# Performance work log

Measured on AMD Instinct MI355X. Metric: run time of the kernel, lower is better.

The kernel has to match this reference:

```python
import jax, jax.numpy as jnp
import numpy as np
from jax import lax

V, E, NL, NS, DC, EX = 32000, 1024, 4, 16, 4, 2
DI = EX * E          # 2048 inner dim
DTR = E // 16        # 64 dt_rank
BSZ, L = 2, 512
EPS = 1e-5


def setup_inputs() -> dict:
    key = jax.random.key(0)
    ks = jax.random.split(key, 12)
    s = 0.02
    emb = jax.random.normal(ks[0], (V, E), jnp.float32) * s
    ln_w = jnp.ones((NL, E), jnp.float32)
    ln_b = jnp.zeros((NL, E), jnp.float32)
    in_proj_w = jax.random.normal(ks[1], (NL, 2 * DI, E), jnp.float32) * s
    conv_w = jax.random.normal(ks[2], (NL, DI, DC), jnp.float32) * 0.1
    conv_b = jnp.zeros((NL, DI), jnp.float32)
    x_proj_w = jax.random.normal(ks[3], (NL, DTR + 2 * NS, DI), jnp.float32) * s
    dt_proj_w = jax.random.normal(ks[4], (NL, DI, DTR), jnp.float32) * s
    dt_proj_b = jax.random.normal(ks[5], (NL, DI), jnp.float32) * 0.1
    # canonical S4D-real init: A[d,n] = n+1  ->  A_log = log(A)
    A_log = jnp.log(jnp.tile(jnp.arange(1, NS + 1, dtype=jnp.float32)[None, None, :], (NL, DI, 1)))
    D_param = jnp.ones((NL, DI), jnp.float32)
    out_proj_w = jax.random.normal(ks[6], (NL, E, DI), jnp.float32) * s
    fln_w = jnp.ones((E,), jnp.float32)
    fln_b = jnp.zeros((E,), jnp.float32)
    input_ids = jax.random.randint(ks[7], (BSZ, L), 0, V, jnp.int64)
    targets = jax.random.randint(ks[8], (BSZ, L), 0, V, jnp.int64)
    return dict(input_ids=input_ids, targets=targets, emb=emb, ln_w=ln_w, ln_b=ln_b,
                in_proj_w=in_proj_w, conv_w=conv_w, conv_b=conv_b, x_proj_w=x_proj_w,
                dt_proj_w=dt_proj_w, dt_proj_b=dt_proj_b, A_log=A_log, D_param=D_param,
                out_proj_w=out_proj_w, fln_w=fln_w, fln_b=fln_b)


def _layer_norm(x, w, b):
    mu = x.mean(-1, keepdims=True)
    var = ((x - mu) ** 2).mean(-1, keepdims=True)
    return (x - mu) * lax.rsqrt(var + EPS) * w + b


def _mamba_block(x, in_w, cw, cb, xw, dtw, dtb, a_log, d_par, ow):
    # x: (B,L,E)
    xz = jnp.einsum('ble,fe->blf', x, in_w)          # (B,L,2*DI)
    u, res = jnp.split(xz, 2, axis=-1)               # each (B,L,DI)
    # causal depthwise conv1d, kernel width DC (left pad DC-1)
    u_pad = jnp.pad(u, ((0, 0), (DC - 1, 0), (0, 0)))
    u_conv = sum(cw[:, k] * u_pad[:, k:k + u.shape[1], :] for k in range(DC))
    u = jax.nn.silu(u_conv + cb)
    x_dbl = jnp.einsum('bld,fd->blf', u, xw)         # (B,L,DTR+2*NS)
    dt = x_dbl[..., :DTR]
    Bm = x_dbl[..., DTR:DTR + NS]                    # (B,L,NS)
    Cm = x_dbl[..., DTR + NS:]                       # (B,L,NS)
    delta = jax.nn.softplus(jnp.einsum('blr,dr->bld', dt, dtw) + dtb)  # (B,L,DI)
    A = -jnp.exp(a_log)                              # (DI,NS)
    dA = jnp.exp(delta[..., None] * A)               # (B,L,DI,NS)
    dBu = delta[..., None] * Bm[:, :, None, :] * u[..., None]

    def step(h, inp):
        dA_t, dBu_t, C_t = inp
        h = dA_t * h + dBu_t                         # (B,DI,NS)
        y = jnp.einsum('bdn,bn->bd', h, C_t)
        return h, y

    h0 = jnp.zeros((x.shape[0], DI, NS), x.dtype)
    _, ys = lax.scan(step, h0, (dA.transpose(1, 0, 2, 3), dBu.transpose(1, 0, 2, 3), Cm.transpose(1, 0, 2)))
    y = ys.transpose(1, 0, 2) + u * d_par            # (B,L,DI)
    y = y * jax.nn.silu(res)
    return jnp.einsum('bld,ed->ble', y, ow)


def reference(input_ids, targets, emb, ln_w, ln_b, in_proj_w, conv_w, conv_b,
              x_proj_w, dt_proj_w, dt_proj_b, A_log, D_param, out_proj_w, fln_w, fln_b):
    x = emb[input_ids]                               # (B,L,E)
    for l in range(NL):
        h = _layer_norm(x, ln_w[l], ln_b[l])
        h = _mamba_block(h, in_proj_w[l], conv_w[l], conv_b[l], x_proj_w[l],
                         dt_proj_w[l], dt_proj_b[l], A_log[l], D_param[l], out_proj_w[l])
        x = x + h
    x = _layer_norm(x, fln_w, fln_b)
    logits = jnp.einsum('ble,ve->blv', x, emb)       # tied lm_head
    logp = jax.nn.log_softmax(logits, axis=-1)
    valid = targets != -1
    safe_t = jnp.where(valid, targets, 0)
    nll = -jnp.take_along_axis(logp, safe_t[..., None], axis=-1)[..., 0]
    loss = jnp.where(valid, nll, 0.0).mean()
    return logits, loss
```

## Files before the change

kernel.cpp:

```cpp
#include <hip/hip_runtime.h>
#include <cstdint>
#include <cstddef>

#define L_SEQ 512
#define NBATCH 2
#define NTOK 1024
#define E_DIM 1024
#define V_DIM 32000
#define DI_DIM 2048
#define NS_DIM 16
#define DTR_DIM 64
#define DC_DIM 4
#define NL_DIM 4
#define NC 8
#define LC (L_SEQ / NC)

typedef __bf16 bf16;
typedef __bf16 bf16x8 __attribute__((ext_vector_type(8)));
typedef __bf16 bf16x4 __attribute__((ext_vector_type(4)));
typedef float  f32x4  __attribute__((ext_vector_type(4)));

__device__ __forceinline__ void gload_lds16(const void* g, void* l)
{
    __builtin_amdgcn_global_load_lds((const __attribute__((address_space(1))) uint32_t*)g,
                                     (__attribute__((address_space(3))) uint32_t*)l, 16, 0, 0);
}

__device__ __forceinline__ float softplusf(float z)
{
    return fmaxf(z, 0.0f) + log1pf(expf(-fabsf(z)));
}

__global__ void cast_f32_to_bf16(const float* __restrict__ in, bf16* __restrict__ out, int n4)
{
    int stride = gridDim.x * blockDim.x;
    for (int i = blockIdx.x * blockDim.x + threadIdx.x; i < n4; i += stride) {
        f32x4 v = ((const f32x4*)in)[i];
        bf16x4 o;
        o[0] = (bf16)v[0]; o[1] = (bf16)v[1]; o[2] = (bf16)v[2]; o[3] = (bf16)v[3];
        ((bf16x4*)out)[i] = o;
    }
}

__global__ void cast3_kernel(const float* __restrict__ a, bf16* __restrict__ oa, int na4,
                             const float* __restrict__ b, bf16* __restrict__ ob, int nb4,
                             const float* __restrict__ c, bf16* __restrict__ oc, int nc4)
{
    int stride = gridDim.x * blockDim.x;
    int tot = na4 + nb4 + nc4;
    for (int i = blockIdx.x * blockDim.x + threadIdx.x; i < tot; i += stride) {
        const float* src; bf16* dst; int k = i;
        if (k < na4) { src = a; dst = oa; }
        else if ((k -= na4) < nb4) { src = b; dst = ob; }
        else { k -= nb4; src = c; dst = oc; }
        f32x4 v = ((const f32x4*)src)[k];
        bf16x4 o;
        o[0] = (bf16)v[0]; o[1] = (bf16)v[1]; o[2] = (bf16)v[2]; o[3] = (bf16)v[3];
        ((bf16x4*)dst)[k] = o;
    }
}

__global__ void embed_kernel(const int* __restrict__ ids, const float* __restrict__ emb,
                             float* __restrict__ x)
{
    int t = blockIdx.x;
    int id = ids[t];
    ((f32x4*)(x + (size_t)t * E_DIM))[threadIdx.x] =
        ((const f32x4*)(emb + (size_t)id * E_DIM))[threadIdx.x];
}

__global__ void ln_kernel(const float* __restrict__ x, const float* __restrict__ w,
                          const float* __restrict__ b, bf16* __restrict__ out)
{
    int t = blockIdx.x;
    int tid = threadIdx.x;
    f32x4 v = ((const f32x4*)(x + (size_t)t * E_DIM))[tid];
    float s  = v[0] + v[1] + v[2] + v[3];
    float sq = v[0]*v[0] + v[1]*v[1] + v[2]*v[2] + v[3]*v[3];
#pragma unroll
    for (int off = 1; off < 64; off <<= 1) { s += __shfl_xor(s, off); sq += __shfl_xor(sq, off); }
    __shared__ float ps[4], pq[4];
    if ((tid & 63) == 0) { ps[tid >> 6] = s; pq[tid >> 6] = sq; }
    __syncthreads();
    float S  = ps[0] + ps[1] + ps[2] + ps[3];
    float SQ = pq[0] + pq[1] + pq[2] + pq[3];
    float mu  = S * (1.0f / E_DIM);
    float var = SQ * (1.0f / E_DIM) - mu * mu;
    float rs  = rsqrtf(var + 1e-5f);
    f32x4 wv = ((const f32x4*)w)[tid];
    f32x4 bv = ((const f32x4*)b)[tid];
    bf16x4 o;
#pragma unroll
    for (int i = 0; i < 4; ++i) o[i] = (bf16)((v[i] - mu) * rs * wv[i] + bv[i]);
    ((bf16x4*)(out + (size_t)t * E_DIM))[tid] = o;
}

template<int BM, int BN, int MODE>
__global__ __launch_bounds__(256) void gemm_bt(const bf16* __restrict__ A, const bf16* __restrict__ B,
                                               void* __restrict__ Cv, int K,
                                               int lda, int ldb, int ldc,
                                               const float* __restrict__ bias,
                                               int RB, int CB, int CBpad)
{
    int pid = blockIdx.x;
    int xcd = pid & 7;
    int j   = pid >> 3;
    int cpx = CBpad >> 3;
    int rb  = j % RB;
    int cb  = xcd * cpx + j / RB;
    if (cb >= CB) return;

    __shared__ __align__(16) bf16 As[BM * 32];
    __shared__ __align__(16) bf16 Bs[BN * 32];
    int tid  = threadIdx.x;
    int lane = tid & 63;
    int wid  = tid >> 6;
    int wr = wid >> 1, wc = wid & 1;
    int li = lane & 15, lg = lane >> 4;
    const bf16* Ablk = A + (size_t)(rb * BM) * lda;
    const bf16* Bblk = B + (size_t)(cb * BN) * ldb;
    constexpr int MR  = BM / 32;
    constexpr int NR  = BN / 32;
    constexpr int TOT = (BM + BN) * 4;
    f32x4 acc[MR][NR] = {};
    for (int k0 = 0; k0 < K; k0 += 32) {
        __syncthreads();
#pragma unroll
        for (int it = 0; it < TOT / 256; ++it) {
            int wbase = it * 256 + wid * 64;
            int idx   = wbase + lane;
            if (wbase < BM * 4) {
                int row = idx >> 2, seg = idx & 3;
                gload_lds16(Ablk + (size_t)row * lda + k0 + seg * 8, As + (size_t)wbase * 8);
            } else {
                int bb  = wbase - BM * 4;
                int bi  = bb + lane;
                int row = bi >> 2, seg = bi & 3;
                gload_lds16(Bblk + (size_t)row * ldb + k0 + seg * 8, Bs + (size_t)bb * 8);
            }
        }
        __syncthreads();
        bf16x8 af[MR], bfr[NR];
#pragma unroll
        for (int m = 0; m < MR; ++m) af[m]  = *(const bf16x8*)&As[(wr * (BM/2) + m * 16 + li) * 32 + lg * 8];
#pragma unroll
        for (int n = 0; n < NR; ++n) bfr[n] = *(const bf16x8*)&Bs[(wc * (BN/2) + n * 16 + li) * 32 + lg * 8];
#pragma unroll
        for (int m = 0; m < MR; ++m)
#pragma unroll
            for (int n = 0; n < NR; ++n)
                acc[m][n] = __builtin_amdgcn_mfma_f32_16x16x32_bf16(af[m], bfr[n], acc[m][n], 0, 0, 0);
    }
    int row0 = rb * BM + wr * (BM/2);
    int col0 = cb * BN + wc * (BN/2);
    float* Cf = (float*)Cv;
    bf16*  Cb = (bf16*)Cv;
#pragma unroll
    for (int m = 0; m < MR; ++m) {
#pragma unroll
        for (int n = 0; n < NR; ++n) {
            int r = row0 + m * 16 + lg * 4;
            int c = col0 + n * 16 + li;
#pragma unroll
            for (int q = 0; q < 4; ++q) {
                float v = acc[m][n][q];
                if (MODE == 0) {
                    Cf[(size_t)(r + q) * ldc + c] = v;
                } else if (MODE == 1) {
                    float* cp = Cf + (size_t)(r + q) * ldc + c;
                    *cp = v + *cp;
                } else if (MODE == 2) {
                    Cb[(size_t)(r + q) * ldc + c] = (bf16)softplusf(v + bias[c]);
                } else if (MODE == 4) {
                    Cb[(size_t)(r + q) * ldc + c] = (bf16)v;
                }
            }
        }
    }
}

template<int BM, int BN, int MODE>
static void launch_gemm(const bf16* A, const bf16* B, void* C, int M, int N, int K,
                        int lda, int ldb, int ldc, const float* bias, hipStream_t stream)
{
    int RB = M / BM;
    int CB = (N + BN - 1) / BN;
    int CBpad = (CB + 7) & ~7;
    gemm_bt<BM, BN, MODE><<<RB * CBpad, 256, 0, stream>>>(A, B, C, K, lda, ldb, ldc,
                                                          bias, RB, CB, CBpad);
}

__global__ __launch_bounds__(256) void cxk_kernel(
        const bf16* __restrict__ xz, const float* __restrict__ cw,
        const float* __restrict__ cb, const float* __restrict__ xw,
        float* __restrict__ xdbl, bf16* __restrict__ dt_bf, bf16* __restrict__ u_bf)
{
    int t0  = blockIdx.x * 2;
    int bb  = t0 >> 9;
    int tid = threadIdx.x;
    int f   = tid & 127;
    int ks  = tid >> 7;
    __shared__ __align__(16) float sxz[5][256];
    __shared__ __align__(16) float su[2][256];
    __shared__ float pacc[2][128];
    float acc[2] = {0, 0};
    for (int kc = 0; kc < DI_DIM; kc += 256) {
        __syncthreads();
#pragma unroll
        for (int it = 0; it < 2; ++it) {
            int idx = it * 256 + tid;
            if (idx < 320) {
                int row = idx >> 6, c4 = (idx & 63) * 4;
                int tr = t0 - 3 + row;
                float v0 = 0, v1 = 0, v2 = 0, v3 = 0;
                if (tr >= bb * L_SEQ) {
                    bf16x4 v = *(const bf16x4*)&xz[(size_t)tr * (2 * DI_DIM) + kc + c4];
                    v0 = (float)v[0]; v1 = (float)v[1]; v2 = (float)v[2]; v3 = (float)v[3];
                }
                sxz[row][c4] = v0; sxz[row][c4 + 1] = v1;
                sxz[row][c4 + 2] = v2; sxz[row][c4 + 3] = v3;
            }
        }
        __syncthreads();
        {
            int c = tid;
            const float* cwp = cw + (size_t)(kc + c) * DC_DIM;
            float w0 = cwp[0], w1 = cwp[1], w2 = cwp[2], w3 = cwp[3];
            float bs = cb[kc + c];
#pragma unroll
            for (int tt = 0; tt < 2; ++tt) {
                float a = bs + w0 * sxz[tt][c] + w1 * sxz[tt + 1][c]
                             + w2 * sxz[tt + 2][c] + w3 * sxz[tt + 3][c];
                float uo = a / (1.0f + __expf(-a));
                su[tt][c] = uo;
                u_bf[(size_t)(t0 + tt) * DI_DIM + kc + c] = (bf16)uo;
            }
        }
        __syncthreads();
        if (f < 96) {
            int kb = ks * 128;
            for (int kk = kb; kk < kb + 128; kk += 4) {
                f32x4 wv = *(const f32x4*)&xw[(size_t)f * DI_DIM + kc + kk];
#pragma unroll
                for (int tt = 0; tt < 2; ++tt) {
                    f32x4 uv = *(f32x4*)&su[tt][kk];
                    acc[tt] += wv[0]*uv[0] + wv[1]*uv[1] + wv[2]*uv[2] + wv[3]*uv[3];
                }
            }
        }
    }
    if (ks == 1 && f < 96) {
#pragma unroll
        for (int tt = 0; tt < 2; ++tt) pacc[tt][f] = acc[tt];
    }
    __syncthreads();
    if (ks == 0 && f < 96) {
#pragma unroll
        for (int tt = 0; tt < 2; ++tt) {
            float v = acc[tt] + pacc[tt][f];
            xdbl[(size_t)(t0 + tt) * 96 + f] = v;
            if (f < 64) dt_bf[(size_t)(t0 + tt) * DTR_DIM + f] = (bf16)v;
        }
    }
}

__global__ __launch_bounds__(256) void scan_phase_a(
        const bf16* __restrict__ delta, const float* __restrict__ xdbl,
        const bf16* __restrict__ u_bf, const float* __restrict__ A_log,
        float* __restrict__ Pbuf, float* __restrict__ Sbuf)
{
    int tid = threadIdx.x;
    int c   = blockIdx.x & (NC - 1);
    int dblk= (blockIdx.x >> 3) & 127;
    int b   = blockIdx.x >> 10;
    int d0  = dblk << 4;
    int n = tid & 15, dl = tid >> 4;
    int d = d0 + dl;
    float Ac = -expf(A_log[(size_t)d * NS_DIM + n]);
    float h = 0.0f, P = 1.0f;
    __shared__ float s_dlt[32][16], s_u[32][16], s_B[32][16];
    int tt0 = tid >> 4, cc = tid & 15;
    int tbase = b * L_SEQ + c * LC;
    for (int t0 = 0; t0 < LC; t0 += 32) {
        __syncthreads();
#pragma unroll
        for (int jj = 0; jj < 2; ++jj) {
            int tt = jj * 16 + tt0;
            size_t trow = (size_t)(tbase + t0 + tt);
            s_dlt[tt][cc] = (float)delta[trow * DI_DIM + d0 + cc];
            s_u[tt][cc]   = (float)u_bf[trow * DI_DIM + d0 + cc];
            s_B[tt][cc]   = xdbl[trow * 96 + 64 + cc];
        }
        __syncthreads();
#pragma unroll
        for (int t = 0; t < 32; ++t) {
            float dlt = s_dlt[t][dl];
            float dA  = __expf(dlt * Ac);
            h = fmaf(dA, h, dlt * s_B[t][n] * s_u[t][dl]);
            P *= dA;
        }
    }
    size_t oi = (((size_t)(b * NC + c) * DI_DIM) + d) * NS_DIM + n;
    Pbuf[oi] = P;
    Sbuf[oi] = h;
}

__global__ void scan_combine(const float* __restrict__ Pbuf, const float* __restrict__ Sbuf,
                             float* __restrict__ Hstart)
{
    int i  = blockIdx.x * 256 + threadIdx.x;
    int b  = i >> 15;
    int dn = i & 32767;
    float h = 0.0f;
#pragma unroll
    for (int c = 0; c < NC; ++c) {
        size_t oi = ((size_t)(b * NC + c) * (DI_DIM * NS_DIM)) + dn;
        Hstart[oi] = h;
        h = fmaf(Pbuf[oi], h, Sbuf[oi]);
    }
}

__global__ __launch_bounds__(256) void scan_phase_c(
        const bf16* __restrict__ delta, const float* __restrict__ xdbl,
        const bf16* __restrict__ u_bf, const bf16* __restrict__ xz,
        const float* __restrict__ A_log, const float* __restrict__ D_par,
        const float* __restrict__ Hstart, bf16* __restrict__ y)
{
    int tid = threadIdx.x;
    int c   = blockIdx.x & (NC - 1);
    int dblk= (blockIdx.x >> 3) & 127;
    int b   = blockIdx.x >> 10;
    int d0  = dblk << 4;
    int n = tid & 15, dl = tid >> 4;
    int d = d0 + dl;
    float Ac = -expf(A_log[(size_t)d * NS_DIM + n]);
    float Dp = D_par[d];
    float h = Hstart[(((size_t)(b * NC + c) * DI_DIM) + d) * NS_DIM + n];
    __shared__ float s_dlt[32][16], s_u[32][16], s_res[32][16], s_B[32][16], s_C[32][16];
    __shared__ bf16  s_y[32][16];
    int tt0 = tid >> 4, cc = tid & 15;
    int tbase = b * L_SEQ + c * LC;
    for (int t0 = 0; t0 < LC; t0 += 32) {
        __syncthreads();
#pragma unroll
        for (int jj = 0; jj < 2; ++jj) {
            int tt = jj * 16 + tt0;
            size_t trow = (size_t)(tbase + t0 + tt);
            s_dlt[tt][cc] = (float)delta[trow * DI_DIM + d0 + cc];
            s_u[tt][cc]   = (float)u_bf[trow * DI_DIM + d0 + cc];
            s_res[tt][cc] = (float)xz[trow * (2 * DI_DIM) + DI_DIM + d0 + cc];
            s_B[tt][cc]   = xdbl[trow * 96 + 64 + cc];
            s_C[tt][cc]   = xdbl[trow * 96 + 80 + cc];
        }
        __syncthreads();
#pragma unroll
        for (int t = 0; t < 32; ++t) {
            float dlt = s_dlt[t][dl];
            float uu  = s_u[t][dl];
            float dA  = __expf(dlt * Ac);
            float dBu = dlt * s_B[t][n] * uu;
            h = fmaf(dA, h, dBu);
            float yp = h * s_C[t][n];
            yp += __shfl_xor(yp, 1);
            yp += __shfl_xor(yp, 2);
            yp += __shfl_xor(yp, 4);
            yp += __shfl_xor(yp, 8);
            if (n == 0) {
                float res = s_res[t][dl];
                float yv  = fmaf(uu, Dp, yp) * (res / (1.0f + __expf(-res)));
                s_y[t][dl] = (bf16)yv;
            }
        }
        __syncthreads();
#pragma unroll
        for (int jj = 0; jj < 2; ++jj) {
            int tt = jj * 16 + tt0;
            size_t trow = (size_t)(tbase + t0 + tt);
            y[trow * DI_DIM + d0 + cc] = s_y[tt][cc];
        }
    }
}

__global__ void lse_nll_kernel(const float* __restrict__ logits, const int* __restrict__ targets,
                               float* __restrict__ lossp)
{
    int t = blockIdx.x, tid = threadIdx.x;
    const f32x4* row = (const f32x4*)(logits + (size_t)t * V_DIM);
    float m = -1e30f, s = 0.0f;
    for (int i = tid; i < V_DIM / 4; i += 256) {
        f32x4 v = row[i];
        float m4 = fmaxf(fmaxf(v[0], v[1]), fmaxf(v[2], v[3]));
        if (m4 > m) { s *= __expf(m - m4); m = m4; }
        s += __expf(v[0] - m) + __expf(v[1] - m) + __expf(v[2] - m) + __expf(v[3] - m);
    }
#pragma unroll
    for (int off = 1; off < 64; off <<= 1) {
        float mo = __shfl_xor(m, off), so = __shfl_xor(s, off);
        float nm = fmaxf(m, mo);
        s = s * __expf(m - nm) + so * __expf(mo - nm);
        m = nm;
    }
    __shared__ float pm[4], ps2[4];
    if ((tid & 63) == 0) { pm[tid >> 6] = m; ps2[tid >> 6] = s; }
    __syncthreads();
    if (tid == 0) {
        float M = fmaxf(fmaxf(pm[0], pm[1]), fmaxf(pm[2], pm[3]));
        float S = ps2[0] * __expf(pm[0] - M) + ps2[1] * __expf(pm[1] - M)
                + ps2[2] * __expf(pm[2] - M) + ps2[3] * __expf(pm[3] - M);
        int tg = targets[t];
        if (tg >= 0) {
            float v = (M + logf(S)) - logits[(size_t)t * V_DIM + tg];
            atomicAdd(lossp, v * (1.0f / NTOK));
        }
    }
}

extern "C" void kernel_launch(void* const* d_in, const int* in_sizes, int n_in,
                              void* d_out, int out_size, void* d_ws, size_t ws_size,
                              hipStream_t stream)
{
    const int*   ids   = (const int*)d_in[0];
    const int*   tgt   = (const int*)d_in[1];
    const float* emb   = (const float*)d_in[2];
    const float* ln_w  = (const float*)d_in[3];
    const float* ln_b  = (const float*)d_in[4];
    const float* inw   = (const float*)d_in[5];
    const float* convw = (const float*)d_in[6];
    const float* convb = (const float*)d_in[7];
    const float* xw    = (const float*)d_in[8];
    const float* dtw   = (const float*)d_in[9];
    const float* dtb   = (const float*)d_in[10];
    const float* alog  = (const float*)d_in[11];
    const float* dpar  = (const float*)d_in[12];
    const float* outw  = (const float*)d_in[13];
    const float* flnw  = (const float*)d_in[14];
    const float* flnb  = (const float*)d_in[15];
    float* logits = (float*)d_out;
    float* lossp  = logits + (size_t)NTOK * V_DIM;

    char* wsp = (char*)d_ws;
    size_t off = 0;
    auto alloc = [&](size_t bytes) -> void* {
        void* p = wsp + off;
        off += (bytes + 255) & ~(size_t)255;
        return p;
    };
    bf16*  emb_bf  = (bf16*)alloc((size_t)V_DIM * E_DIM * 2);
    bf16*  winl    = (bf16*)alloc((size_t)2 * DI_DIM * E_DIM * 2);
    bf16*  woutl   = (bf16*)alloc((size_t)E_DIM * DI_DIM * 2);
    bf16*  wdtl    = (bf16*)alloc((size_t)DI_DIM * DTR_DIM * 2);
    float* x       = (float*)alloc((size_t)NTOK * E_DIM * 4);
    bf16*  h_bf    = (bf16*)alloc((size_t)NTOK * E_DIM * 2);
    bf16*  xzb     = (bf16*)alloc((size_t)NTOK * 2 * DI_DIM * 2);
    bf16*  u_bf    = (bf16*)alloc((size_t)NTOK * DI_DIM * 2);
    float* xdbl    = (float*)alloc((size_t)NTOK * 96 * 4);
    bf16*  dt_bf   = (bf16*)alloc((size_t)NTOK * DTR_DIM * 2);
    bf16*  deltab  = (bf16*)alloc((size_t)NTOK * DI_DIM * 2);
    bf16*  y_bf    = (bf16*)alloc((size_t)NTOK * DI_DIM * 2);
    bf16*  xf_bf   = (bf16*)alloc((size_t)NTOK * E_DIM * 2);
    float* Pbuf    = (float*)alloc((size_t)NBATCH * NC * DI_DIM * NS_DIM * 4);
    float* Sbuf    = (float*)alloc((size_t)NBATCH * NC * DI_DIM * NS_DIM * 4);
    float* Hstart  = (float*)alloc((size_t)NBATCH * NC * DI_DIM * NS_DIM * 4);
    if (off > ws_size) return;

    hipMemsetAsync(lossp, 0, sizeof(float), stream);
    {
        int n4 = (int)((size_t)V_DIM * E_DIM / 4);
        cast_f32_to_bf16<<<4096, 256, 0, stream>>>(emb, emb_bf, n4);
    }
    embed_kernel<<<NTOK, 256, 0, stream>>>(ids, emb, x);

    for (int l = 0; l < NL_DIM; ++l) {
        cast3_kernel<<<2048, 256, 0, stream>>>(
            inw  + (size_t)l * 2 * DI_DIM * E_DIM, winl,  (int)((size_t)2 * DI_DIM * E_DIM / 4),
            outw + (size_t)l * E_DIM * DI_DIM,     woutl, (int)((size_t)E_DIM * DI_DIM / 4),
            dtw  + (size_t)l * DI_DIM * DTR_DIM,   wdtl,  (int)((size_t)DI_DIM * DTR_DIM / 4));

        ln_kernel<<<NTOK, 256, 0, stream>>>(x, ln_w + l * E_DIM, ln_b + l * E_DIM, h_bf);
        launch_gemm<128, 64, 4>(h_bf, winl, xzb, NTOK, 2 * DI_DIM, E_DIM,
                                E_DIM, E_DIM, 2 * DI_DIM, nullptr, stream);
        cxk_kernel<<<NTOK / 2, 256, 0, stream>>>(
            xzb, convw + (size_t)l * DI_DIM * DC_DIM, convb + (size_t)l * DI_DIM,
            xw + (size_t)l * 96 * DI_DIM, xdbl, dt_bf, u_bf);
        launch_gemm<64, 64, 2>(dt_bf, wdtl, deltab, NTOK, DI_DIM, DTR_DIM,
                               DTR_DIM, DTR_DIM, DI_DIM, dtb + (size_t)l * DI_DIM, stream);
        scan_phase_a<<<NBATCH * (DI_DIM / 16) * NC, 256, 0, stream>>>(
            deltab, xdbl, u_bf, alog + (size_t)l * DI_DIM * NS_DIM, Pbuf, Sbuf);
        scan_combine<<<NBATCH * DI_DIM * NS_DIM / 256, 256, 0, stream>>>(Pbuf, Sbuf, Hstart);
        scan_phase_c<<<NBATCH * (DI_DIM / 16) * NC, 256, 0, stream>>>(
            deltab, xdbl, u_bf, xzb, alog + (size_t)l * DI_DIM * NS_DIM,
            dpar + (size_t)l * DI_DIM, Hstart, y_bf);
        launch_gemm<64, 64, 1>(y_bf, woutl, x, NTOK, E_DIM, DI_DIM,
                               DI_DIM, DI_DIM, E_DIM, nullptr, stream);
    }
    ln_kernel<<<NTOK, 256, 0, stream>>>(x, flnw, flnb, xf_bf);
    launch_gemm<128, 128, 0>(xf_bf, emb_bf, logits, NTOK, V_DIM, E_DIM,
                             E_DIM, E_DIM, V_DIM, nullptr, stream);
    lse_nll_kernel<<<NTOK, 256, 0, stream>>>(logits, tgt, lossp);
}
```

Measured before the change: 921.5 us.

## Split-K out_proj with atomics, fold scan combine into phase C, widen conv tile

```diff
diff --git a/kernel.cpp b/kernel.cpp
--- a/kernel.cpp
+++ b/kernel.cpp
@@ -95,7 +95,7 @@
     ((bf16x4*)(out + (size_t)t * E_DIM))[tid] = o;
 }
 
-template<int BM, int BN, int MODE>
+template<int BM, int BN, int MODE, int SK>
 __global__ __launch_bounds__(256) void gemm_bt(const bf16* __restrict__ A, const bf16* __restrict__ B,
                                                void* __restrict__ Cv, int K,
                                                int lda, int ldb, int ldc,
@@ -103,12 +103,18 @@
                                                int RB, int CB, int CBpad)
 {
     int pid = blockIdx.x;
-    int xcd = pid & 7;
-    int j   = pid >> 3;
+    int per = RB * CBpad;
+    int sk  = pid / per;
+    int rem = pid - sk * per;
+    int xcd = rem & 7;
+    int j   = rem >> 3;
     int cpx = CBpad >> 3;
     int rb  = j % RB;
     int cb  = xcd * cpx + j / RB;
     if (cb >= CB) return;
+    int kseg = K / SK;
+    int kbeg = sk * kseg;
+    int kend = kbeg + kseg;
 
     __shared__ __align__(16) bf16 As[BM * 32];
     __shared__ __align__(16) bf16 Bs[BN * 32];
@@ -123,7 +129,7 @@
     constexpr int NR  = BN / 32;
     constexpr int TOT = (BM + BN) * 4;
     f32x4 acc[MR][NR] = {};
-    for (int k0 = 0; k0 < K; k0 += 32) {
+    for (int k0 = kbeg; k0 < kend; k0 += 32) {
         __syncthreads();
 #pragma unroll
         for (int it = 0; it < TOT / 256; ++it) {
@@ -173,21 +179,23 @@
                     Cb[(size_t)(r + q) * ldc + c] = (bf16)softplusf(v + bias[c]);
                 } else if (MODE == 4) {
                     Cb[(size_t)(r + q) * ldc + c] = (bf16)v;
+                } else if (MODE == 5) {
+                    atomicAdd(Cf + (size_t)(r + q) * ldc + c, v);
                 }
             }
         }
     }
 }
 
-template<int BM, int BN, int MODE>
+template<int BM, int BN, int MODE, int SK = 1>
 static void launch_gemm(const bf16* A, const bf16* B, void* C, int M, int N, int K,
                         int lda, int ldb, int ldc, const float* bias, hipStream_t stream)
 {
     int RB = M / BM;
     int CB = (N + BN - 1) / BN;
     int CBpad = (CB + 7) & ~7;
-    gemm_bt<BM, BN, MODE><<<RB * CBpad, 256, 0, stream>>>(A, B, C, K, lda, ldb, ldc,
-                                                          bias, RB, CB, CBpad);
+    gemm_bt<BM, BN, MODE, SK><<<RB * CBpad * SK, 256, 0, stream>>>(A, B, C, K, lda, ldb, ldc,
+                                                                   bias, RB, CB, CBpad);
 }
 
 __global__ __launch_bounds__(256) void cxk_kernel(
@@ -195,31 +203,28 @@
         const float* __restrict__ cb, const float* __restrict__ xw,
         float* __restrict__ xdbl, bf16* __restrict__ dt_bf, bf16* __restrict__ u_bf)
 {
-    int t0  = blockIdx.x * 2;
+    int t0  = blockIdx.x * 4;
     int bb  = t0 >> 9;
     int tid = threadIdx.x;
     int f   = tid & 127;
     int ks  = tid >> 7;
-    __shared__ __align__(16) float sxz[5][256];
-    __shared__ __align__(16) float su[2][256];
-    __shared__ float pacc[2][128];
-    float acc[2] = {0, 0};
+    __shared__ __align__(16) float sxz[7][256];
+    __shared__ __align__(16) float su[4][256];
+    __shared__ float pacc[4][128];
+    float acc[4] = {0, 0, 0, 0};
     for (int kc = 0; kc < DI_DIM; kc += 256) {
         __syncthreads();
-#pragma unroll
-        for (int it = 0; it < 2; ++it) {
-            int idx = it * 256 + tid;
-            if (idx < 320) {
-                int row = idx >> 6, c4 = (idx & 63) * 4;
-                int tr = t0 - 3 + row;
-                float v0 = 0, v1 = 0, v2 = 0, v3 = 0;
-                if (tr >= bb * L_SEQ) {
-                    bf16x4 v = *(const bf16x4*)&xz[(size_t)tr * (2 * DI_DIM) + kc + c4];
-                    v0 = (float)v[0]; v1 = (float)v[1]; v2 = (float)v[2]; v3 = (float)v[3];
-                }
-                sxz[row][c4] = v0; sxz[row][c4 + 1] = v1;
-                sxz[row][c4 + 2] = v2; sxz[row][c4 + 3] = v3;
-            }
+        if (tid < 224) {
+            int row = tid >> 5, c8 = (tid & 31) * 8;
+            int tr = t0 - 3 + row;
+            float vals[8] = {0, 0, 0, 0, 0, 0, 0, 0};
+            if (tr >= bb * L_SEQ) {
+                bf16x8 v = *(const bf16x8*)&xz[(size_t)tr * (2 * DI_DIM) + kc + c8];
+#pragma unroll
+                for (int jj = 0; jj < 8; ++jj) vals[jj] = (float)v[jj];
+            }
+#pragma unroll
+            for (int jj = 0; jj < 8; ++jj) sxz[row][c8 + jj] = vals[jj];
         }
         __syncthreads();
         {
@@ -228,7 +233,7 @@
             float w0 = cwp[0], w1 = cwp[1], w2 = cwp[2], w3 = cwp[3];
             float bs = cb[kc + c];
 #pragma unroll
-            for (int tt = 0; tt < 2; ++tt) {
+            for (int tt = 0; tt < 4; ++tt) {
                 float a = bs + w0 * sxz[tt][c] + w1 * sxz[tt + 1][c]
                              + w2 * sxz[tt + 2][c] + w3 * sxz[tt + 3][c];
                 float uo = a / (1.0f + __expf(-a));
@@ -242,7 +247,7 @@
             for (int kk = kb; kk < kb + 128; kk += 4) {
                 f32x4 wv = *(const f32x4*)&xw[(size_t)f * DI_DIM + kc + kk];
 #pragma unroll
-                for (int tt = 0; tt < 2; ++tt) {
+                for (int tt = 0; tt < 4; ++tt) {
                     f32x4 uv = *(f32x4*)&su[tt][kk];
                     acc[tt] += wv[0]*uv[0] + wv[1]*uv[1] + wv[2]*uv[2] + wv[3]*uv[3];
                 }
@@ -251,12 +256,12 @@
     }
     if (ks == 1 && f < 96) {
 #pragma unroll
-        for (int tt = 0; tt < 2; ++tt) pacc[tt][f] = acc[tt];
+        for (int tt = 0; tt < 4; ++tt) pacc[tt][f] = acc[tt];
     }
     __syncthreads();
     if (ks == 0 && f < 96) {
 #pragma unroll
-        for (int tt = 0; tt < 2; ++tt) {
+        for (int tt = 0; tt < 4; ++tt) {
             float v = acc[tt] + pacc[tt][f];
             xdbl[(size_t)(t0 + tt) * 96 + f] = v;
             if (f < 64) dt_bf[(size_t)(t0 + tt) * DTR_DIM + f] = (bf16)v;
@@ -305,26 +310,12 @@
     Sbuf[oi] = h;
 }
 
-__global__ void scan_combine(const float* __restrict__ Pbuf, const float* __restrict__ Sbuf,
-                             float* __restrict__ Hstart)
-{
-    int i  = blockIdx.x * 256 + threadIdx.x;
-    int b  = i >> 15;
-    int dn = i & 32767;
-    float h = 0.0f;
-#pragma unroll
-    for (int c = 0; c < NC; ++c) {
-        size_t oi = ((size_t)(b * NC + c) * (DI_DIM * NS_DIM)) + dn;
-        Hstart[oi] = h;
-        h = fmaf(Pbuf[oi], h, Sbuf[oi]);
-    }
-}
-
 __global__ __launch_bounds__(256) void scan_phase_c(
         const bf16* __restrict__ delta, const float* __restrict__ xdbl,
         const bf16* __restrict__ u_bf, const bf16* __restrict__ xz,
         const float* __restrict__ A_log, const float* __restrict__ D_par,
-        const float* __restrict__ Hstart, bf16* __restrict__ y)
+        const float* __restrict__ Pbuf, const float* __restrict__ Sbuf,
+        bf16* __restrict__ y)
 {
     int tid = threadIdx.x;
     int c   = blockIdx.x & (NC - 1);
@@ -335,7 +326,11 @@
     int d = d0 + dl;
     float Ac = -expf(A_log[(size_t)d * NS_DIM + n]);
     float Dp = D_par[d];
-    float h = Hstart[(((size_t)(b * NC + c) * DI_DIM) + d) * NS_DIM + n];
+    float h = 0.0f;
+    for (int cp = 0; cp < c; ++cp) {
+        size_t oi = (((size_t)(b * NC + cp) * DI_DIM) + d) * NS_DIM + n;
+        h = fmaf(Pbuf[oi], h, Sbuf[oi]);
+    }
     __shared__ float s_dlt[32][16], s_u[32][16], s_res[32][16], s_B[32][16], s_C[32][16];
     __shared__ bf16  s_y[32][16];
     int tt0 = tid >> 4, cc = tid & 15;
@@ -460,7 +455,6 @@
     bf16*  xf_bf   = (bf16*)alloc((size_t)NTOK * E_DIM * 2);
     float* Pbuf    = (float*)alloc((size_t)NBATCH * NC * DI_DIM * NS_DIM * 4);
     float* Sbuf    = (float*)alloc((size_t)NBATCH * NC * DI_DIM * NS_DIM * 4);
-    float* Hstart  = (float*)alloc((size_t)NBATCH * NC * DI_DIM * NS_DIM * 4);
     if (off > ws_size) return;
 
     hipMemsetAsync(lossp, 0, sizeof(float), stream);
@@ -479,19 +473,18 @@
         ln_kernel<<<NTOK, 256, 0, stream>>>(x, ln_w + l * E_DIM, ln_b + l * E_DIM, h_bf);
         launch_gemm<128, 64, 4>(h_bf, winl, xzb, NTOK, 2 * DI_DIM, E_DIM,
                                 E_DIM, E_DIM, 2 * DI_DIM, nullptr, stream);
-        cxk_kernel<<<NTOK / 2, 256, 0, stream>>>(
+        cxk_kernel<<<NTOK / 4, 256, 0, stream>>>(
             xzb, convw + (size_t)l * DI_DIM * DC_DIM, convb + (size_t)l * DI_DIM,
             xw + (size_t)l * 96 * DI_DIM, xdbl, dt_bf, u_bf);
         launch_gemm<64, 64, 2>(dt_bf, wdtl, deltab, NTOK, DI_DIM, DTR_DIM,
                                DTR_DIM, DTR_DIM, DI_DIM, dtb + (size_t)l * DI_DIM, stream);
         scan_phase_a<<<NBATCH * (DI_DIM / 16) * NC, 256, 0, stream>>>(
             deltab, xdbl, u_bf, alog + (size_t)l * DI_DIM * NS_DIM, Pbuf, Sbuf);
-        scan_combine<<<NBATCH * DI_DIM * NS_DIM / 256, 256, 0, stream>>>(Pbuf, Sbuf, Hstart);
         scan_phase_c<<<NBATCH * (DI_DIM / 16) * NC, 256, 0, stream>>>(
             deltab, xdbl, u_bf, xzb, alog + (size_t)l * DI_DIM * NS_DIM,
-            dpar + (size_t)l * DI_DIM, Hstart, y_bf);
-        launch_gemm<64, 64, 1>(y_bf, woutl, x, NTOK, E_DIM, DI_DIM,
-                               DI_DIM, DI_DIM, E_DIM, nullptr, stream);
+            dpar + (size_t)l * DI_DIM, Pbuf, Sbuf, y_bf);
+        launch_gemm<128, 128, 5, 4>(y_bf, woutl, x, NTOK, E_DIM, DI_DIM,
+                                    DI_DIM, DI_DIM, E_DIM, nullptr, stream);
     }
     ln_kernel<<<NTOK, 256, 0, stream>>>(x, flnw, flnb, xf_bf);
     launch_gemm<128, 128, 0>(xf_bf, emb_bf, logits, NTOK, V_DIM, E_DIM,
```

Measured after the change: 852.4 us. -7.5%, faster.
